# Kernel optimization log

Hardware: AMD Instinct MI355X
Metric: run time of the kernel (lower is better)

## Reference

```python
import jax, jax.numpy as jnp
import numpy as np

N = 50000      # nodes
E = 800000     # edges (before self-loops)
IN_DIM = 128
HID = 32
HEADS = 8
OUT_DIM = 16
NEG_SLOPE = 0.2  # PyG GATConv default


def setup_inputs() -> dict:
    key = jax.random.key(0)
    ks = jax.random.split(key, 12)
    x = jax.random.normal(ks[0], (N, IN_DIM), dtype=jnp.float32)
    edge_index = jax.random.randint(ks[1], (2, E), 0, N, dtype=jnp.int32)
    s = 0.1
    # layer 1: GATConv(IN_DIM -> HID, heads=HEADS, concat=True)
    W1 = jax.random.normal(ks[2], (IN_DIM, HEADS * HID), dtype=jnp.float32) * s
    a_src1 = jax.random.normal(ks[3], (HEADS, HID), dtype=jnp.float32) * s
    a_dst1 = jax.random.normal(ks[4], (HEADS, HID), dtype=jnp.float32) * s
    b1 = jax.random.normal(ks[5], (HEADS * HID,), dtype=jnp.float32) * s
    # layer 2: GATConv(HEADS*HID -> HID, heads=1, concat=True)
    W2 = jax.random.normal(ks[6], (HEADS * HID, HID), dtype=jnp.float32) * s
    a_src2 = jax.random.normal(ks[7], (1, HID), dtype=jnp.float32) * s
    a_dst2 = jax.random.normal(ks[8], (1, HID), dtype=jnp.float32) * s
    b2 = jax.random.normal(ks[9], (HID,), dtype=jnp.float32) * s
    # output Linear(HID -> OUT_DIM)
    Wout = jax.random.normal(ks[10], (HID, OUT_DIM), dtype=jnp.float32) * s
    bout = jax.random.normal(ks[11], (OUT_DIM,), dtype=jnp.float32) * s
    return {"x": x, "edge_index": edge_index, "W1": W1, "a_src1": a_src1,
            "a_dst1": a_dst1, "b1": b1, "W2": W2, "a_src2": a_src2,
            "a_dst2": a_dst2, "b2": b2, "Wout": Wout, "bout": bout}


def _gat_conv(x, src, dst, W, a_src, a_dst, b, num_nodes):
    """PyG GATConv (eval mode): linear proj, edge attention logits,
    segment-softmax over incoming edges per dst node, weighted scatter-sum.
    src/dst already include self-loops. Returns [N, H, D]."""
    H, D = a_src.shape
    h = (x @ W).reshape(num_nodes, H, D)                 # [N,H,D]
    alpha_s = jnp.einsum('nhd,hd->nh', h, a_src)         # [N,H]
    alpha_d = jnp.einsum('nhd,hd->nh', h, a_dst)         # [N,H]
    e = jax.nn.leaky_relu(alpha_s[src] + alpha_d[dst], NEG_SLOPE)  # [Etot,H]
    # numerically-stable segment softmax over edges grouped by dst
    m = jax.ops.segment_max(e, dst, num_segments=num_nodes)        # [N,H]
    ex = jnp.exp(e - m[dst])
    den = jax.ops.segment_sum(ex, dst, num_segments=num_nodes)     # [N,H]
    alpha = ex / (den[dst] + 1e-16)                                 # [Etot,H]
    out = jax.ops.segment_sum(alpha[:, :, None] * h[src], dst,
                              num_segments=num_nodes)               # [N,H,D]
    return out, b


def reference(x, edge_index, W1, a_src1, a_dst1, b1, W2, a_src2, a_dst2, b2,
              Wout, bout):
    n = x.shape[0]
    loop = jnp.arange(n, dtype=edge_index.dtype)
    src = jnp.concatenate([edge_index[0], loop])  # PyG add_self_loops=True
    dst = jnp.concatenate([edge_index[1], loop])
    o1, _ = _gat_conv(x, src, dst, W1, a_src1, a_dst1, b1, n)
    h1 = jax.nn.elu(o1.reshape(n, -1) + b1)       # concat heads -> [N, H*D]
    o2, _ = _gat_conv(h1, src, dst, W2, a_src2, a_dst2, b2, n)
    h2 = jax.nn.elu(o2.reshape(n, -1) + b2)       # heads=1 -> [N, HID]
    return h2 @ Wout + bout                        # [N, OUT_DIM]
```

## Files before the change

kernel.cpp:

```cpp
#include <hip/hip_runtime.h>
#include <math.h>

#define IN_DIM 128
#define HID 32
#define HEADS 8
#define OUT_DIM 16
#define NEG_SLOPE 0.2f


__global__ void count_kernel(const int* __restrict__ ei, int* __restrict__ counts,
                             int E, int N) {
    int e = blockIdx.x * 256 + threadIdx.x;
    int Etot = E + N;
    if (e >= Etot) return;
    int dst = (e < E) ? ei[E + e] : (e - E);
    atomicAdd(&counts[dst], 1);
}

__global__ __launch_bounds__(1024) void scan_kernel(const int* __restrict__ counts,
                                                    int* __restrict__ off,
                                                    int* __restrict__ pos, int N) {
    __shared__ int wsum[16];
    __shared__ int wbase[16];
    __shared__ int running_s;
    int tid = threadIdx.x;
    int lane = tid & 63, wid = tid >> 6;
    if (tid == 0) running_s = 0;
    __syncthreads();
    const int CH = 4096;
    int nchunk = (N + CH - 1) / CH;
    for (int c = 0; c < nchunk; ++c) {
        int base_i = c * CH + tid * 4;
        int v0 = (base_i + 0 < N) ? counts[base_i + 0] : 0;
        int v1 = (base_i + 1 < N) ? counts[base_i + 1] : 0;
        int v2 = (base_i + 2 < N) ? counts[base_i + 2] : 0;
        int v3 = (base_i + 3 < N) ? counts[base_i + 3] : 0;
        int tsum = v0 + v1 + v2 + v3;
        int x = tsum;
        #pragma unroll
        for (int ofs = 1; ofs < 64; ofs <<= 1) {
            int y = __shfl_up(x, ofs, 64);
            if (lane >= ofs) x += y;
        }
        if (lane == 63) wsum[wid] = x;
        __syncthreads();
        if (wid == 0) {
            int w = (lane < 16) ? wsum[lane] : 0;
            #pragma unroll
            for (int ofs = 1; ofs < 64; ofs <<= 1) {
                int y = __shfl_up(w, ofs, 64);
                if (lane >= ofs) w += y;
            }
            if (lane < 16) wbase[lane] = w;
        }
        __syncthreads();
        int chunk_base = running_s;
        int wave_excl = (wid == 0) ? 0 : wbase[wid - 1];
        int thr_excl = x - tsum;
        int b = chunk_base + wave_excl + thr_excl;
        if (base_i + 0 < N) { off[base_i + 0] = b; pos[base_i + 0] = b; } b += v0;
        if (base_i + 1 < N) { off[base_i + 1] = b; pos[base_i + 1] = b; } b += v1;
        if (base_i + 2 < N) { off[base_i + 2] = b; pos[base_i + 2] = b; } b += v2;
        if (base_i + 3 < N) { off[base_i + 3] = b; pos[base_i + 3] = b; }
        __syncthreads();
        if (tid == 0) running_s = chunk_base + wbase[15];
        __syncthreads();
    }
    if (tid == 0) off[N] = running_s;
}

__global__ void fill_kernel(const int* __restrict__ ei, int* __restrict__ pos,
                            int* __restrict__ csr_src, int E, int N) {
    int e = blockIdx.x * 256 + threadIdx.x;
    int Etot = E + N;
    if (e >= Etot) return;
    int src, dst;
    if (e < E) { src = ei[e]; dst = ei[E + e]; }
    else       { src = e - E; dst = e - E; }
    int idx = atomicAdd(&pos[dst], 1);
    csr_src[idx] = src;
}

__global__ __launch_bounds__(256) void gemm1_kernel(const float* __restrict__ x,
                                                    const float* __restrict__ W,
                                                    float* __restrict__ hp, int N) {
    __shared__ float xs[32 * IN_DIM];
    int n0 = blockIdx.x * 32;
    int t = threadIdx.x;
    int rows = min(32, N - n0);
    const float4* xg = (const float4*)(x + (size_t)n0 * IN_DIM);
    float4* xs4 = (float4*)xs;
    int nf4 = rows * (IN_DIM / 4);
    for (int idx = t; idx < 32 * (IN_DIM / 4); idx += 256) {
        float4 v = (idx < nf4) ? xg[idx] : make_float4(0.f, 0.f, 0.f, 0.f);
        xs4[idx] = v;
    }
    __syncthreads();
    float acc[32];
    #pragma unroll
    for (int i = 0; i < 32; ++i) acc[i] = 0.f;
    for (int k4 = 0; k4 < IN_DIM / 4; ++k4) {
        int k = k4 * 4;
        float w0 = W[(k + 0) * 256 + t];
        float w1 = W[(k + 1) * 256 + t];
        float w2 = W[(k + 2) * 256 + t];
        float w3 = W[(k + 3) * 256 + t];
        #pragma unroll
        for (int i = 0; i < 32; ++i) {
            float4 xv = xs4[i * (IN_DIM / 4) + k4];
            acc[i] += xv.x * w0 + xv.y * w1 + xv.z * w2 + xv.w * w3;
        }
    }
    for (int i = 0; i < rows; ++i)
        hp[(size_t)(n0 + i) * 256 + t] = acc[i];
}

__global__ void alpha1_kernel(const float* __restrict__ hp,
                              const float* __restrict__ a_src,
                              const float* __restrict__ a_dst,
                              float* __restrict__ as, float* __restrict__ ad, int NH) {
    int t = blockIdx.x * 256 + threadIdx.x;
    if (t >= NH) return;
    int h = t & 7;
    const float4* hv  = (const float4*)(hp + (size_t)t * 32);
    const float4* av  = (const float4*)(a_src + h * 32);
    const float4* bv  = (const float4*)(a_dst + h * 32);
    float ss = 0.f, sd = 0.f;
    #pragma unroll
    for (int k = 0; k < 8; ++k) {
        float4 xv = hv[k], a = av[k], b = bv[k];
        ss += xv.x * a.x + xv.y * a.y + xv.z * a.z + xv.w * a.w;
        sd += xv.x * b.x + xv.y * b.y + xv.z * b.z + xv.w * b.w;
    }
    as[t] = ss;
    ad[t] = sd;
}

__global__ __launch_bounds__(256) void attn1_kernel(const int* __restrict__ off,
                                                    const int* __restrict__ csr_src,
                                                    const float* __restrict__ as,
                                                    const float* __restrict__ ad,
                                                    const float* __restrict__ hp,
                                                    const float* __restrict__ bias,
                                                    float* __restrict__ out, int N) {
    __shared__ float sred[4][8];
    __shared__ float ws[32][8];
    __shared__ int   ss[32];
    int n = blockIdx.x;
    int t = threadIdx.x;
    int wid = t >> 6, lane = t & 63;
    int beg = off[n], end = off[n + 1];
    int h8 = t & 7;
    int ie = t >> 3;
    float adn = ad[n * 8 + h8];

    float m = -INFINITY;
    for (int i = beg + ie; i < end; i += 32) {
        float e = as[csr_src[i] * 8 + h8] + adn;
        e = (e > 0.f) ? e : NEG_SLOPE * e;
        m = fmaxf(m, e);
    }
    m = fmaxf(m, __shfl_xor(m, 8, 64));
    m = fmaxf(m, __shfl_xor(m, 16, 64));
    m = fmaxf(m, __shfl_xor(m, 32, 64));
    if (lane < 8) sred[wid][lane] = m;
    __syncthreads();
    m = fmaxf(fmaxf(sred[0][h8], sred[1][h8]), fmaxf(sred[2][h8], sred[3][h8]));
    __syncthreads();

    float den = 0.f;
    for (int i = beg + ie; i < end; i += 32) {
        float e = as[csr_src[i] * 8 + h8] + adn;
        e = (e > 0.f) ? e : NEG_SLOPE * e;
        den += expf(e - m);
    }
    den += __shfl_xor(den, 8, 64);
    den += __shfl_xor(den, 16, 64);
    den += __shfl_xor(den, 32, 64);
    if (lane < 8) sred[wid][lane] = den;
    __syncthreads();
    den = sred[0][h8] + sred[1][h8] + sred[2][h8] + sred[3][h8];
    float inv = 1.f / (den + 1e-16f);

    int hh = t >> 5;
    float acc = 0.f;
    for (int c0 = beg; c0 < end; c0 += 32) {
        int i = c0 + ie;
        float w = 0.f; int s = 0;
        if (i < end) {
            s = csr_src[i];
            float e = as[s * 8 + h8] + adn;
            e = (e > 0.f) ? e : NEG_SLOPE * e;
            w = expf(e - m) * inv;
        }
        __syncthreads();
        ws[ie][h8] = w;
        if (h8 == 0) ss[ie] = s;
        __syncthreads();
        int cnt = min(32, end - c0);
        for (int j = 0; j < cnt; ++j)
            acc += ws[j][hh] * hp[(size_t)ss[j] * 256 + t];
    }
    float v = acc + bias[t];
    out[(size_t)n * 256 + t] = (v > 0.f) ? v : expm1f(v);
}

__global__ __launch_bounds__(256) void gemm2_kernel(const float* __restrict__ h1,
                                                    const float* __restrict__ W2,
                                                    float* __restrict__ hp2, int N) {
    __shared__ float hs[8 * 256];
    int n0 = blockIdx.x * 8;
    int t = threadIdx.x;
    int rows = min(8, N - n0);
    const float4* hg = (const float4*)(h1 + (size_t)n0 * 256);
    float4* hs4 = (float4*)hs;
    int nf4 = rows * 64;
    for (int idx = t; idx < 512; idx += 256)
        hs4[idx] = (idx < nf4) ? hg[idx] : make_float4(0.f, 0.f, 0.f, 0.f);
    __syncthreads();
    int i = t >> 5, j = t & 31;
    const float4* hrow = (const float4*)(hs + i * 256);
    float acc = 0.f;
    for (int k4 = 0; k4 < 64; ++k4) {
        float4 hv = hrow[k4];
        int k = k4 * 4;
        acc += hv.x * W2[(k + 0) * 32 + j] + hv.y * W2[(k + 1) * 32 + j]
             + hv.z * W2[(k + 2) * 32 + j] + hv.w * W2[(k + 3) * 32 + j];
    }
    if (i < rows) hp2[(size_t)(n0 + i) * 32 + j] = acc;
}

__global__ void alpha2_kernel(const float* __restrict__ hp2,
                              const float* __restrict__ a_src,
                              const float* __restrict__ a_dst,
                              float* __restrict__ as, float* __restrict__ ad, int N) {
    int t = blockIdx.x * 256 + threadIdx.x;
    if (t >= N) return;
    const float4* hv = (const float4*)(hp2 + (size_t)t * 32);
    const float4* av = (const float4*)a_src;
    const float4* bv = (const float4*)a_dst;
    float ss = 0.f, sd = 0.f;
    #pragma unroll
    for (int k = 0; k < 8; ++k) {
        float4 xv = hv[k], a = av[k], b = bv[k];
        ss += xv.x * a.x + xv.y * a.y + xv.z * a.z + xv.w * a.w;
        sd += xv.x * b.x + xv.y * b.y + xv.z * b.z + xv.w * b.w;
    }
    as[t] = ss;
    ad[t] = sd;
}

__global__ __launch_bounds__(256) void attn2_kernel(const int* __restrict__ off,
                                                    const int* __restrict__ csr_src,
                                                    const float* __restrict__ as,
                                                    const float* __restrict__ ad,
                                                    const float* __restrict__ hp2,
                                                    const float* __restrict__ b2,
                                                    float* __restrict__ h2, int N) {
    int g = threadIdx.x >> 5, d = threadIdx.x & 31;
    int n = blockIdx.x * 8 + g;
    if (n >= N) return;
    int beg = off[n], end = off[n + 1];
    float adn = ad[n];

    float m = -INFINITY;
    for (int i = beg + d; i < end; i += 32) {
        float e = as[csr_src[i]] + adn;
        e = (e > 0.f) ? e : NEG_SLOPE * e;
        m = fmaxf(m, e);
    }
    #pragma unroll
    for (int mask = 16; mask >= 1; mask >>= 1) m = fmaxf(m, __shfl_xor(m, mask, 32));

    float den = 0.f;
    for (int i = beg + d; i < end; i += 32) {
        float e = as[csr_src[i]] + adn;
        e = (e > 0.f) ? e : NEG_SLOPE * e;
        den += expf(e - m);
    }
    #pragma unroll
    for (int mask = 16; mask >= 1; mask >>= 1) den += __shfl_xor(den, mask, 32);
    float inv = 1.f / (den + 1e-16f);

    float acc = 0.f;
    for (int c0 = beg; c0 < end; c0 += 32) {
        int i = c0 + d;
        float w = 0.f; int s = 0;
        if (i < end) {
            s = csr_src[i];
            float e = as[s] + adn;
            e = (e > 0.f) ? e : NEG_SLOPE * e;
            w = expf(e - m) * inv;
        }
        int cnt = min(32, end - c0);
        for (int j = 0; j < cnt; ++j) {
            float wj = __shfl(w, j, 32);
            int   sj = __shfl(s, j, 32);
            acc += wj * hp2[(size_t)sj * 32 + d];
        }
    }
    float v = acc + b2[d];
    h2[(size_t)n * 32 + d] = (v > 0.f) ? v : expm1f(v);
}

__global__ void out_kernel(const float* __restrict__ h2,
                           const float* __restrict__ Wout,
                           const float* __restrict__ bout,
                           float* __restrict__ out, int N) {
    int t = blockIdx.x * 256 + threadIdx.x;
    if (t >= N * OUT_DIM) return;
    int n = t >> 4, j = t & 15;
    const float* hr = h2 + (size_t)n * 32;
    float acc = bout[j];
    #pragma unroll
    for (int k = 0; k < 32; ++k)
        acc += hr[k] * Wout[k * OUT_DIM + j];
    out[t] = acc;
}


extern "C" void kernel_launch(void* const* d_in, const int* in_sizes, int n_in,
                              void* d_out, int out_size, void* d_ws, size_t ws_size,
                              hipStream_t stream) {
    const float* x      = (const float*)d_in[0];
    const int*   ei     = (const int*)d_in[1];
    const float* W1     = (const float*)d_in[2];
    const float* a_src1 = (const float*)d_in[3];
    const float* a_dst1 = (const float*)d_in[4];
    const float* b1     = (const float*)d_in[5];
    const float* W2     = (const float*)d_in[6];
    const float* a_src2 = (const float*)d_in[7];
    const float* a_dst2 = (const float*)d_in[8];
    const float* b2     = (const float*)d_in[9];
    const float* Wout   = (const float*)d_in[10];
    const float* bout   = (const float*)d_in[11];
    float* out = (float*)d_out;

    const int N = in_sizes[0] / IN_DIM;
    const int E = in_sizes[1] / 2;
    const int Etot = E + N;

    char* p = (char*)d_ws;
    auto alloc = [&](size_t bytes) -> void* {
        void* r = (void*)p;
        p += (bytes + 255) & ~(size_t)255;
        return r;
    };
    float* hp1    = (float*)alloc((size_t)N * 256 * 4);
    float* h1     = (float*)alloc((size_t)N * 256 * 4);
    float* as1    = (float*)alloc((size_t)N * 8 * 4);
    float* ad1    = (float*)alloc((size_t)N * 8 * 4);
    float* hp2    = (float*)alloc((size_t)N * 32 * 4);
    float* as2    = (float*)alloc((size_t)N * 4);
    float* ad2    = (float*)alloc((size_t)N * 4);
    float* h2     = (float*)alloc((size_t)N * 32 * 4);
    int*   counts = (int*)alloc((size_t)N * 4);
    int*   off    = (int*)alloc((size_t)(N + 1) * 4);
    int*   pos    = (int*)alloc((size_t)N * 4);
    int*   csr    = (int*)alloc((size_t)Etot * 4);
    (void)ws_size;

    hipMemsetAsync(counts, 0, (size_t)N * 4, stream);
    int eb = (Etot + 255) / 256;
    count_kernel<<<eb, 256, 0, stream>>>(ei, counts, E, N);
    scan_kernel<<<1, 1024, 0, stream>>>(counts, off, pos, N);
    fill_kernel<<<eb, 256, 0, stream>>>(ei, pos, csr, E, N);

    gemm1_kernel<<<(N + 31) / 32, 256, 0, stream>>>(x, W1, hp1, N);
    alpha1_kernel<<<(N * 8 + 255) / 256, 256, 0, stream>>>(hp1, a_src1, a_dst1, as1, ad1, N * 8);
    attn1_kernel<<<N, 256, 0, stream>>>(off, csr, as1, ad1, hp1, b1, h1, N);

    gemm2_kernel<<<(N + 7) / 8, 256, 0, stream>>>(h1, W2, hp2, N);
    alpha2_kernel<<<(N + 255) / 256, 256, 0, stream>>>(hp2, a_src2, a_dst2, as2, ad2, N);
    attn2_kernel<<<(N + 7) / 8, 256, 0, stream>>>(off, csr, as2, ad2, hp2, b2, h2, N);

    out_kernel<<<(N * OUT_DIM + 255) / 256, 256, 0, stream>>>(h2, Wout, bout, out, N);
}
```

Measured before the change: 571.8 us.

## Fuse softmax denominator into aggregation pass and register-tile gemm1 with float4

Both attention kernels drop the separate denominator pass over the edges. The exp sum is accumulated during the weighted aggregation pass and the normalisation is applied once at the end, which removes one gather sweep over csr_src and the alpha arrays. gemm1 is re-tiled so each thread computes an 8-row by 4-column float4 block with vectorised W loads and stores, instead of 32 rows by 1 column. attn1 also uses readfirstlane to keep the source index scalar, at the cost of an extra pair of syncs for the reduction at the end.

Result: slower. 616.1 us (+7.7%).

```diff
diff --git a/kernel.cpp b/kernel.cpp
--- a/kernel.cpp
+++ b/kernel.cpp
@@ -84,35 +84,43 @@
 __global__ __launch_bounds__(256) void gemm1_kernel(const float* __restrict__ x,
                                                     const float* __restrict__ W,
                                                     float* __restrict__ hp, int N) {
-    __shared__ float xs[32 * IN_DIM];
+    __shared__ float4 xs4[32 * 32];
     int n0 = blockIdx.x * 32;
     int t = threadIdx.x;
     int rows = min(32, N - n0);
     const float4* xg = (const float4*)(x + (size_t)n0 * IN_DIM);
-    float4* xs4 = (float4*)xs;
-    int nf4 = rows * (IN_DIM / 4);
-    for (int idx = t; idx < 32 * (IN_DIM / 4); idx += 256) {
-        float4 v = (idx < nf4) ? xg[idx] : make_float4(0.f, 0.f, 0.f, 0.f);
-        xs4[idx] = v;
-    }
-    __syncthreads();
-    float acc[32];
-    #pragma unroll
-    for (int i = 0; i < 32; ++i) acc[i] = 0.f;
-    for (int k4 = 0; k4 < IN_DIM / 4; ++k4) {
-        int k = k4 * 4;
-        float w0 = W[(k + 0) * 256 + t];
-        float w1 = W[(k + 1) * 256 + t];
-        float w2 = W[(k + 2) * 256 + t];
-        float w3 = W[(k + 3) * 256 + t];
+    int nf4 = rows * 32;
+    for (int idx = t; idx < 1024; idx += 256)
+        xs4[idx] = (idx < nf4) ? xg[idx] : make_float4(0.f, 0.f, 0.f, 0.f);
+    __syncthreads();
+
+    int c4 = t & 63;
+    int r0 = (t >> 6) * 8;
+    const float4* W4 = (const float4*)W;
+    float4 acc[8];
+    #pragma unroll
+    for (int i = 0; i < 8; ++i) acc[i] = make_float4(0.f, 0.f, 0.f, 0.f);
+
+    #pragma unroll 4
+    for (int k4 = 0; k4 < 32; ++k4) {
+        float4 w0 = W4[(k4 * 4 + 0) * 64 + c4];
+        float4 w1 = W4[(k4 * 4 + 1) * 64 + c4];
+        float4 w2 = W4[(k4 * 4 + 2) * 64 + c4];
+        float4 w3 = W4[(k4 * 4 + 3) * 64 + c4];
         #pragma unroll
-        for (int i = 0; i < 32; ++i) {
-            float4 xv = xs4[i * (IN_DIM / 4) + k4];
-            acc[i] += xv.x * w0 + xv.y * w1 + xv.z * w2 + xv.w * w3;
-        }
-    }
-    for (int i = 0; i < rows; ++i)
-        hp[(size_t)(n0 + i) * 256 + t] = acc[i];
+        for (int i = 0; i < 8; ++i) {
+            float4 xq = xs4[(r0 + i) * 32 + k4];
+            acc[i].x += xq.x * w0.x + xq.y * w1.x + xq.z * w2.x + xq.w * w3.x;
+            acc[i].y += xq.x * w0.y + xq.y * w1.y + xq.z * w2.y + xq.w * w3.y;
+            acc[i].z += xq.x * w0.z + xq.y * w1.z + xq.z * w2.z + xq.w * w3.z;
+            acc[i].w += xq.x * w0.w + xq.y * w1.w + xq.z * w2.w + xq.w * w3.w;
+        }
+    }
+    float4* hp4 = (float4*)hp;
+    #pragma unroll
+    for (int i = 0; i < 8; ++i)
+        if (r0 + i < rows)
+            hp4[(size_t)(n0 + r0 + i) * 64 + c4] = acc[i];
 }
 
 __global__ void alpha1_kernel(const float* __restrict__ hp,
@@ -146,6 +154,7 @@
     __shared__ float sred[4][8];
     __shared__ float ws[32][8];
     __shared__ int   ss[32];
+    __shared__ float sinv[8];
     int n = blockIdx.x;
     int t = threadIdx.x;
     int wid = t >> 6, lane = t & 63;
@@ -168,22 +177,10 @@
     m = fmaxf(fmaxf(sred[0][h8], sred[1][h8]), fmaxf(sred[2][h8], sred[3][h8]));
     __syncthreads();
 
-    float den = 0.f;
-    for (int i = beg + ie; i < end; i += 32) {
-        float e = as[csr_src[i] * 8 + h8] + adn;
-        e = (e > 0.f) ? e : NEG_SLOPE * e;
-        den += expf(e - m);
-    }
-    den += __shfl_xor(den, 8, 64);
-    den += __shfl_xor(den, 16, 64);
-    den += __shfl_xor(den, 32, 64);
-    if (lane < 8) sred[wid][lane] = den;
-    __syncthreads();
-    den = sred[0][h8] + sred[1][h8] + sred[2][h8] + sred[3][h8];
-    float inv = 1.f / (den + 1e-16f);
-
     int hh = t >> 5;
+    float den_part = 0.f;
     float acc = 0.f;
+    const float* hpt = hp + t;
     for (int c0 = beg; c0 < end; c0 += 32) {
         int i = c0 + ie;
         float w = 0.f; int s = 0;
@@ -191,17 +188,30 @@
             s = csr_src[i];
             float e = as[s * 8 + h8] + adn;
             e = (e > 0.f) ? e : NEG_SLOPE * e;
-            w = expf(e - m) * inv;
-        }
+            w = expf(e - m);
+        }
+        den_part += w;
         __syncthreads();
         ws[ie][h8] = w;
         if (h8 == 0) ss[ie] = s;
         __syncthreads();
         int cnt = min(32, end - c0);
-        for (int j = 0; j < cnt; ++j)
-            acc += ws[j][hh] * hp[(size_t)ss[j] * 256 + t];
-    }
-    float v = acc + bias[t];
+        for (int j = 0; j < cnt; ++j) {
+            int sj = __builtin_amdgcn_readfirstlane(ss[j]);
+            acc += ws[j][hh] * hpt[(size_t)sj * 256];
+        }
+    }
+    den_part += __shfl_xor(den_part, 8, 64);
+    den_part += __shfl_xor(den_part, 16, 64);
+    den_part += __shfl_xor(den_part, 32, 64);
+    if (lane < 8) sred[wid][lane] = den_part;
+    __syncthreads();
+    if (t < 8) {
+        float den = sred[0][t] + sred[1][t] + sred[2][t] + sred[3][t];
+        sinv[t] = 1.f / (den + 1e-16f);
+    }
+    __syncthreads();
+    float v = acc * sinv[hh] + bias[t];
     out[(size_t)n * 256 + t] = (v > 0.f) ? v : expm1f(v);
 }
 
@@ -272,16 +282,7 @@
     #pragma unroll
     for (int mask = 16; mask >= 1; mask >>= 1) m = fmaxf(m, __shfl_xor(m, mask, 32));
 
-    float den = 0.f;
-    for (int i = beg + d; i < end; i += 32) {
-        float e = as[csr_src[i]] + adn;
-        e = (e > 0.f) ? e : NEG_SLOPE * e;
-        den += expf(e - m);
-    }
-    #pragma unroll
-    for (int mask = 16; mask >= 1; mask >>= 1) den += __shfl_xor(den, mask, 32);
-    float inv = 1.f / (den + 1e-16f);
-
+    float den_part = 0.f;
     float acc = 0.f;
     for (int c0 = beg; c0 < end; c0 += 32) {
         int i = c0 + d;
@@ -290,8 +291,9 @@
             s = csr_src[i];
             float e = as[s] + adn;
             e = (e > 0.f) ? e : NEG_SLOPE * e;
-            w = expf(e - m) * inv;
-        }
+            w = expf(e - m);
+        }
+        den_part += w;
         int cnt = min(32, end - c0);
         for (int j = 0; j < cnt; ++j) {
             float wj = __shfl(w, j, 32);
@@ -299,7 +301,11 @@
             acc += wj * hp2[(size_t)sj * 32 + d];
         }
     }
-    float v = acc + b2[d];
+    #pragma unroll
+    for (int mask = 16; mask >= 1; mask >>= 1) den_part += __shfl_xor(den_part, mask, 32);
+    float inv = 1.f / (den_part + 1e-16f);
+
+    float v = acc * inv + b2[d];
     h2[(size_t)n * 32 + d] = (v > 0.f) ? v : expm1f(v);
 }
 
```
